# Kernel optimization log

Measured on AMD Instinct MI355X. Metric: run time of the kernel, lower is better.

The kernel has to match this reference:

```python
import jax, jax.numpy as jnp
import numpy as np

N_RUNS, T, N_AGENTS, SENSING = 128, 2048, 16, 7
HIDDEN, OUT = 22, 2


def setup_inputs() -> dict:
    key = jax.random.key(0)
    k_runs, k_comm, k_w1, k_b1, k_w2, k_b2 = jax.random.split(key, 6)
    runs = jax.random.normal(k_runs, (N_RUNS, T, N_AGENTS, SENSING), dtype=jnp.float32)
    # init_comm: zero boundary pads, uniform(0,1) interior, one vector per run
    comm_init = jax.random.uniform(k_comm, (N_RUNS, N_AGENTS + 2), dtype=jnp.float32)
    comm_init = comm_init.at[:, 0].set(0.0).at[:, -1].set(0.0)
    W1 = jax.random.normal(k_w1, (HIDDEN, SENSING + 2), dtype=jnp.float32) * (1.0 / np.sqrt(SENSING + 2))
    b1 = jax.random.normal(k_b1, (HIDDEN,), dtype=jnp.float32) * 0.01
    W2 = jax.random.normal(k_w2, (OUT, HIDDEN), dtype=jnp.float32) * (1.0 / np.sqrt(HIDDEN))
    b2 = jax.random.normal(k_b2, (OUT,), dtype=jnp.float32) * 0.01
    return {"runs": runs, "comm_init": comm_init, "W1": W1, "b1": b1, "W2": W2, "b2": b2}


def reference(runs, comm_init, W1, b1, W2, b2):
    # Sync.sequential: agents processed in index order; agent i reads comm[i]
    # (freshly written by agent i-1) and comm[i+2], then writes comm[i+1].
    n_agents = runs.shape[2]

    def agent_step(carry, i):
        comm, xs_t = carry  # comm: [N+2], xs_t: [N, 7]
        inp = jnp.concatenate([xs_t[i], jnp.stack([comm[i], comm[i + 2]])])  # [9]
        h = jax.nn.relu(W1 @ inp + b1)
        out = W2 @ h + b2  # [2]: (control, new_comm)
        comm = comm.at[i + 1].set(out[1])
        return (comm, xs_t), out[0]

    def time_step(comm, xs_t):
        (comm, _), controls = jax.lax.scan(agent_step, (comm, xs_t), jnp.arange(n_agents))
        return comm, controls  # controls: [N]

    def run_fn(run, comm0):
        # comm persists across timesteps within a run
        _, controls = jax.lax.scan(time_step, comm0, run)
        return controls  # [T, N]

    return jax.vmap(run_fn)(runs, comm_init)  # [n_runs, T, N]
```

## Files before the change

### kernel.cpp

```cpp
#include <hip/hip_runtime.h>

#define NRUNS  128
#define TSTEPS 2048
#define NAG    16
#define SENS   7
#define HID    22

typedef float float2v __attribute__((ext_vector_type(2)));

template<int CTRL>
__device__ __forceinline__ float dpp_mov(float v) {
    return __int_as_float(__builtin_amdgcn_update_dpp(
        0, __float_as_int(v), CTRL, 0xf, 0xf, true));
}

__device__ __forceinline__ float grp_reduce(float v) {
    v += dpp_mov<0xB1>(v);
    v += dpp_mov<0x4E>(v);
    v += dpp_mov<0x141>(v);
    return v;
}

__device__ __forceinline__ float bperm(int byteaddr, float v) {
    return __int_as_float(__builtin_amdgcn_ds_bpermute(byteaddr, __float_as_int(v)));
}

struct RawBlk { float2v v[4][7]; };
struct XpBlk  { float e[4][3]; float o[4][3]; };

__global__ void __launch_bounds__(64, 1) comm_net_kernel(
    const float* __restrict__ runs,
    const float* __restrict__ comm_init,
    const float* __restrict__ W1,
    const float* __restrict__ b1,
    const float* __restrict__ W2,
    const float* __restrict__ b2,
    float* __restrict__ out)
{
    const int run  = blockIdx.x;
    const int lane = threadIdx.x & 63;
    const int g    = lane >> 3;
    const int sub  = lane & 7;
    const bool g0  = (g == 0);
    const bool g7  = (g == 7);

    float w1x[3][SENS], wA[3], wB[3], b1v[3], w20[3], w21[3];
#pragma unroll
    for (int u = 0; u < 3; ++u) {
        int j = sub * 3 + u;
        bool valid = (j < HID);
        int jj = valid ? j : 0;
        float m = valid ? 1.0f : 0.0f;
#pragma unroll
        for (int k = 0; k < SENS; ++k) w1x[u][k] = m * W1[jj * 9 + k];
        wA[u]  = m * W1[jj * 9 + 7];
        wB[u]  = m * W1[jj * 9 + 8];
        b1v[u] = m * b1[jj];
        w20[u] = m * W2[jj];
        w21[u] = m * W2[HID + jj];
    }
    const float b20 = b2[0], b21 = b2[1];

    const int addr_even = ((lane - 8) & 63) * 4;
    const int addr_odd  = ((lane + 8) & 63) * 4;

    const float* ci = comm_init + run * (NAG + 2);
    float prevV = ci[2 * g + 2];
    const float initV_e = ci[2 * g + 1];
    const float initV_o = ci[2 * g + 2];

    const float* pr = runs + (size_t)run * TSTEPS * NAG * SENS;
    float*       po = out  + (size_t)run * TSTEPS * NAG;

    auto xpart_pair = [&](const float2v (&r)[7], float (&ae)[3], float (&ao)[3]) {
#pragma unroll
        for (int u = 0; u < 3; ++u) {
            float e = b1v[u];
            e = fmaf(w1x[u][0], r[0].x, e);
            e = fmaf(w1x[u][1], r[0].y, e);
            e = fmaf(w1x[u][2], r[1].x, e);
            e = fmaf(w1x[u][3], r[1].y, e);
            e = fmaf(w1x[u][4], r[2].x, e);
            e = fmaf(w1x[u][5], r[2].y, e);
            e = fmaf(w1x[u][6], r[3].x, e);
            ae[u] = e;
            float o = b1v[u];
            o = fmaf(w1x[u][0], r[3].y, o);
            o = fmaf(w1x[u][1], r[4].x, o);
            o = fmaf(w1x[u][2], r[4].y, o);
            o = fmaf(w1x[u][3], r[5].x, o);
            o = fmaf(w1x[u][4], r[5].y, o);
            o = fmaf(w1x[u][5], r[6].x, o);
            o = fmaf(w1x[u][6], r[6].y, o);
            ao[u] = o;
        }
    };

    auto substep_even = [&](float xe0, float xe1, float xe2, float& o0out) {
        float cross = bperm(addr_even, prevV);
        float cL = g0 ? 0.f : cross;
        float a0 = fmaxf(fmaf(wA[0], cL, fmaf(wB[0], prevV, xe0)), 0.f);
        float a1 = fmaxf(fmaf(wA[1], cL, fmaf(wB[1], prevV, xe1)), 0.f);
        float a2 = fmaxf(fmaf(wA[2], cL, fmaf(wB[2], prevV, xe2)), 0.f);
        float p0 = w20[0] * a0; p0 = fmaf(w20[1], a1, p0); p0 = fmaf(w20[2], a2, p0);
        float p1 = w21[0] * a0; p1 = fmaf(w21[1], a1, p1); p1 = fmaf(w21[2], a2, p1);
        o0out = grp_reduce(p0) + b20;
        prevV = grp_reduce(p1) + b21;
    };
    auto substep_odd = [&](float xo0, float xo1, float xo2, float& o0out) {
        float cross = bperm(addr_odd, prevV);
        float cR = g7 ? 0.f : cross;
        float a0 = fmaxf(fmaf(wB[0], cR, fmaf(wA[0], prevV, xo0)), 0.f);
        float a1 = fmaxf(fmaf(wB[1], cR, fmaf(wA[1], prevV, xo1)), 0.f);
        float a2 = fmaxf(fmaf(wB[2], cR, fmaf(wA[2], prevV, xo2)), 0.f);
        float p0 = w20[0] * a0; p0 = fmaf(w20[1], a1, p0); p0 = fmaf(w20[2], a2, p0);
        float p1 = w21[0] * a0; p1 = fmaf(w21[1], a1, p1); p1 = fmaf(w21[2], a2, p1);
        o0out = grp_reduce(p0) + b20;
        prevV = grp_reduce(p1) + b21;
    };

    auto ramp_pair = [&](int s) {
        int t  = (s >> 1) - g;
        int tc = t < 0 ? 0 : (t > TSTEPS - 1 ? TSTEPS - 1 : t);
        const float2v* xp = (const float2v*)(pr + ((size_t)tc * NAG + 2 * g) * SENS);
        float2v r[7];
#pragma unroll
        for (int k = 0; k < 7; ++k) r[k] = xp[k];
        float ae[3], ao[3];
        xpart_pair(r, ae, ao);
        bool inr = (t >= 0) && (t < TSTEPS);
        float o0;
        substep_even(ae[0], ae[1], ae[2], o0);
        if (inr) po[(size_t)t * NAG + 2 * g] = o0;
        prevV = (t < 0) ? initV_e : prevV;
        substep_odd(ao[0], ao[1], ao[2], o0);
        if (inr) po[(size_t)t * NAG + 2 * g + 1] = o0;
        prevV = (t < 0) ? initV_o : prevV;
    };

#pragma unroll 1
    for (int s = 0; s <= 14; s += 2) ramp_pair(s);

    const float2v* xv = (const float2v*)(pr + ((size_t)(8 - g) * NAG + 2 * g) * SENS);
    float* oe = po + (size_t)(8 - g) * NAG + 2 * g;

    RawBlk RA, RB;
    XpBlk  P0, P1;

    auto load_blk = [&](RawBlk& R, const float2v* p) {
#pragma unroll
        for (int j = 0; j < 4; ++j)
#pragma unroll
            for (int k = 0; k < 7; ++k)
                R.v[j][k] = p[j * 56 + k];
    };
    auto xpart_blk = [&](XpBlk& P, const RawBlk& R) {
#pragma unroll
        for (int j = 0; j < 4; ++j) xpart_pair(R.v[j], P.e[j], P.o[j]);
    };
    auto process_blk = [&](const XpBlk& P) {
#pragma unroll
        for (int j = 0; j < 4; ++j) {
            float o0;
            substep_even(P.e[j][0], P.e[j][1], P.e[j][2], o0);
            oe[0] = o0;
            substep_odd(P.o[j][0], P.o[j][1], P.o[j][2], o0);
            oe[1] = o0;
            oe += NAG;
        }
    };

    load_blk(RA, xv);
    load_blk(RB, xv + 224);
    xpart_blk(P0, RA);
    load_blk(RA, xv + 2 * 224);

#pragma unroll 1
    for (int bm = 0; bm < 506; bm += 2) {
        xpart_blk(P1, RB);
        load_blk(RB, xv + (size_t)(bm + 3) * 224);
        process_blk(P0);
        xpart_blk(P0, RA);
        load_blk(RA, xv + (size_t)(bm + 4) * 224);
        process_blk(P1);
    }
    xpart_blk(P1, RB);
    load_blk(RB, xv + (size_t)509 * 224);
    process_blk(P0);
    xpart_blk(P0, RA);
    process_blk(P1);
    xpart_blk(P1, RB);
    process_blk(P0);
    process_blk(P1);

#pragma unroll 1
    for (int s = 2 * TSTEPS; s <= 2 * TSTEPS + 12; s += 2) ramp_pair(s);
}

extern "C" void kernel_launch(void* const* d_in, const int* in_sizes, int n_in,
                              void* d_out, int out_size, void* d_ws, size_t ws_size,
                              hipStream_t stream) {
    const float* runs      = (const float*)d_in[0];
    const float* comm_init = (const float*)d_in[1];
    const float* W1        = (const float*)d_in[2];
    const float* b1        = (const float*)d_in[3];
    const float* W2        = (const float*)d_in[4];
    const float* b2        = (const float*)d_in[5];
    float* out = (float*)d_out;

    dim3 grid(NRUNS), block(64);
    hipLaunchKernelGGL(comm_net_kernel, grid, block, 0, stream,
                       runs, comm_init, W1, b1, W2, b2, out);
}
```

Measured before the change: 456.4 us.

## Remap lanes to agent-major layout with packed float2 math and permlane reductions

```diff
diff --git a/kernel.cpp b/kernel.cpp
--- a/kernel.cpp
+++ b/kernel.cpp
@@ -14,19 +14,15 @@
         0, __float_as_int(v), CTRL, 0xf, 0xf, true));
 }
 
-__device__ __forceinline__ float grp_reduce(float v) {
-    v += dpp_mov<0xB1>(v);
-    v += dpp_mov<0x4E>(v);
-    v += dpp_mov<0x141>(v);
-    return v;
-}
-
-__device__ __forceinline__ float bperm(int byteaddr, float v) {
-    return __int_as_float(__builtin_amdgcn_ds_bpermute(byteaddr, __float_as_int(v)));
-}
-
-struct RawBlk { float2v v[4][7]; };
-struct XpBlk  { float e[4][3]; float o[4][3]; };
+__device__ __forceinline__ float grp_sum(float v) {
+    v += dpp_mov<0x128>(v);
+    unsigned u = __float_as_uint(v);
+    auto r = __builtin_amdgcn_permlane32_swap(u, u, false, false);
+    return __uint_as_float(r[0]) + __uint_as_float(r[1]);
+}
+
+struct RawBlk { float2v v[2][7]; };
+struct XpBlk  { float2v e[2][3]; float2v o[2][3]; };
 
 __global__ void __launch_bounds__(64, 1) comm_net_kernel(
     const float* __restrict__ runs,
@@ -39,30 +35,34 @@
 {
     const int run  = blockIdx.x;
     const int lane = threadIdx.x & 63;
-    const int g    = lane >> 3;
-    const int sub  = lane & 7;
-    const bool g0  = (g == 0);
-    const bool g7  = (g == 7);
-
-    float w1x[3][SENS], wA[3], wB[3], b1v[3], w20[3], w21[3];
-#pragma unroll
-    for (int u = 0; u < 3; ++u) {
-        int j = sub * 3 + u;
-        bool valid = (j < HID);
-        int jj = valid ? j : 0;
-        float m = valid ? 1.0f : 0.0f;
-#pragma unroll
-        for (int k = 0; k < SENS; ++k) w1x[u][k] = m * W1[jj * 9 + k];
-        wA[u]  = m * W1[jj * 9 + 7];
-        wB[u]  = m * W1[jj * 9 + 8];
-        b1v[u] = m * b1[jj];
-        w20[u] = m * W2[jj];
-        w21[u] = m * W2[HID + jj];
+    const int g    = lane & 7;
+    const int sub2 = ((lane >> 3) & 1) | ((lane >> 4) & 2);
+    const bool g0 = (g == 0);
+    const bool g7 = (g == 7);
+
+    float2v w1p[3][SENS], b1p[3], wAp[3], wAmp[3], wBp[3], wBmp[3], w20p[3], w21p[3];
+#pragma unroll
+    for (int u2 = 0; u2 < 3; ++u2) {
+#pragma unroll
+        for (int h = 0; h < 2; ++h) {
+            int j = sub2 * 6 + u2 * 2 + h;
+            bool valid = (j < HID);
+            int jj = valid ? j : 0;
+            float m = valid ? 1.0f : 0.0f;
+#pragma unroll
+            for (int k = 0; k < SENS; ++k) w1p[u2][k][h] = m * W1[jj * 9 + k];
+            float wa = m * W1[jj * 9 + 7];
+            float wb = m * W1[jj * 9 + 8];
+            wAp[u2][h]  = wa;
+            wAmp[u2][h] = g0 ? 0.f : wa;
+            wBp[u2][h]  = wb;
+            wBmp[u2][h] = g7 ? 0.f : wb;
+            b1p[u2][h]  = m * b1[jj];
+            w20p[u2][h] = m * W2[jj];
+            w21p[u2][h] = m * W2[HID + jj];
+        }
     }
     const float b20 = b2[0], b21 = b2[1];
-
-    const int addr_even = ((lane - 8) & 63) * 4;
-    const int addr_odd  = ((lane + 8) & 63) * 4;
 
     const float* ci = comm_init + run * (NAG + 2);
     float prevV = ci[2 * g + 2];
@@ -72,51 +72,57 @@
     const float* pr = runs + (size_t)run * TSTEPS * NAG * SENS;
     float*       po = out  + (size_t)run * TSTEPS * NAG;
 
-    auto xpart_pair = [&](const float2v (&r)[7], float (&ae)[3], float (&ao)[3]) {
-#pragma unroll
-        for (int u = 0; u < 3; ++u) {
-            float e = b1v[u];
-            e = fmaf(w1x[u][0], r[0].x, e);
-            e = fmaf(w1x[u][1], r[0].y, e);
-            e = fmaf(w1x[u][2], r[1].x, e);
-            e = fmaf(w1x[u][3], r[1].y, e);
-            e = fmaf(w1x[u][4], r[2].x, e);
-            e = fmaf(w1x[u][5], r[2].y, e);
-            e = fmaf(w1x[u][6], r[3].x, e);
-            ae[u] = e;
-            float o = b1v[u];
-            o = fmaf(w1x[u][0], r[3].y, o);
-            o = fmaf(w1x[u][1], r[4].x, o);
-            o = fmaf(w1x[u][2], r[4].y, o);
-            o = fmaf(w1x[u][3], r[5].x, o);
-            o = fmaf(w1x[u][4], r[5].y, o);
-            o = fmaf(w1x[u][5], r[6].x, o);
-            o = fmaf(w1x[u][6], r[6].y, o);
-            ao[u] = o;
+    auto xpart_pair = [&](const float2v (&r)[7], float2v (&ae)[3], float2v (&ao)[3]) {
+#pragma unroll
+        for (int u2 = 0; u2 < 3; ++u2) {
+            float2v e = b1p[u2];
+            e = w1p[u2][0] * (float2v){r[0].x, r[0].x} + e;
+            e = w1p[u2][1] * (float2v){r[0].y, r[0].y} + e;
+            e = w1p[u2][2] * (float2v){r[1].x, r[1].x} + e;
+            e = w1p[u2][3] * (float2v){r[1].y, r[1].y} + e;
+            e = w1p[u2][4] * (float2v){r[2].x, r[2].x} + e;
+            e = w1p[u2][5] * (float2v){r[2].y, r[2].y} + e;
+            e = w1p[u2][6] * (float2v){r[3].x, r[3].x} + e;
+            ae[u2] = e;
+            float2v o = b1p[u2];
+            o = w1p[u2][0] * (float2v){r[3].y, r[3].y} + o;
+            o = w1p[u2][1] * (float2v){r[4].x, r[4].x} + o;
+            o = w1p[u2][2] * (float2v){r[4].y, r[4].y} + o;
+            o = w1p[u2][3] * (float2v){r[5].x, r[5].x} + o;
+            o = w1p[u2][4] * (float2v){r[5].y, r[5].y} + o;
+            o = w1p[u2][5] * (float2v){r[6].x, r[6].x} + o;
+            o = w1p[u2][6] * (float2v){r[6].y, r[6].y} + o;
+            ao[u2] = o;
         }
     };
 
-    auto substep_even = [&](float xe0, float xe1, float xe2, float& o0out) {
-        float cross = bperm(addr_even, prevV);
-        float cL = g0 ? 0.f : cross;
-        float a0 = fmaxf(fmaf(wA[0], cL, fmaf(wB[0], prevV, xe0)), 0.f);
-        float a1 = fmaxf(fmaf(wA[1], cL, fmaf(wB[1], prevV, xe1)), 0.f);
-        float a2 = fmaxf(fmaf(wA[2], cL, fmaf(wB[2], prevV, xe2)), 0.f);
-        float p0 = w20[0] * a0; p0 = fmaf(w20[1], a1, p0); p0 = fmaf(w20[2], a2, p0);
-        float p1 = w21[0] * a0; p1 = fmaf(w21[1], a1, p1); p1 = fmaf(w21[2], a2, p1);
-        o0out = grp_reduce(p0) + b20;
-        prevV = grp_reduce(p1) + b21;
-    };
-    auto substep_odd = [&](float xo0, float xo1, float xo2, float& o0out) {
-        float cross = bperm(addr_odd, prevV);
-        float cR = g7 ? 0.f : cross;
-        float a0 = fmaxf(fmaf(wB[0], cR, fmaf(wA[0], prevV, xo0)), 0.f);
-        float a1 = fmaxf(fmaf(wB[1], cR, fmaf(wA[1], prevV, xo1)), 0.f);
-        float a2 = fmaxf(fmaf(wB[2], cR, fmaf(wA[2], prevV, xo2)), 0.f);
-        float p0 = w20[0] * a0; p0 = fmaf(w20[1], a1, p0); p0 = fmaf(w20[2], a2, p0);
-        float p1 = w21[0] * a0; p1 = fmaf(w21[1], a1, p1); p1 = fmaf(w21[2], a2, p1);
-        o0out = grp_reduce(p0) + b20;
-        prevV = grp_reduce(p1) + b21;
+    auto substep_even = [&](const float2v (&xe)[3], float& o0out) {
+        float cL = dpp_mov<0x111>(prevV);
+        float2v cL2 = {cL, cL}, pV2 = {prevV, prevV};
+        float2v a0 = wAmp[0] * cL2 + (wBp[0] * pV2 + xe[0]);
+        float2v a1 = wAmp[1] * cL2 + (wBp[1] * pV2 + xe[1]);
+        float2v a2 = wAmp[2] * cL2 + (wBp[2] * pV2 + xe[2]);
+        a0.x = fmaxf(a0.x, 0.f); a0.y = fmaxf(a0.y, 0.f);
+        a1.x = fmaxf(a1.x, 0.f); a1.y = fmaxf(a1.y, 0.f);
+        a2.x = fmaxf(a2.x, 0.f); a2.y = fmaxf(a2.y, 0.f);
+        float2v q0 = w20p[0] * a0; q0 = w20p[1] * a1 + q0; q0 = w20p[2] * a2 + q0;
+        float2v q1 = w21p[0] * a0; q1 = w21p[1] * a1 + q1; q1 = w21p[2] * a2 + q1;
+        o0out = grp_sum(q0.x + q0.y) + b20;
+        prevV = grp_sum(q1.x + q1.y) + b21;
+    };
+    auto substep_odd = [&](const float2v (&xo)[3], float& o0out) {
+        float cR = dpp_mov<0x101>(prevV);
+        float2v cR2 = {cR, cR}, pV2 = {prevV, prevV};
+        float2v a0 = wBmp[0] * cR2 + (wAp[0] * pV2 + xo[0]);
+        float2v a1 = wBmp[1] * cR2 + (wAp[1] * pV2 + xo[1]);
+        float2v a2 = wBmp[2] * cR2 + (wAp[2] * pV2 + xo[2]);
+        a0.x = fmaxf(a0.x, 0.f); a0.y = fmaxf(a0.y, 0.f);
+        a1.x = fmaxf(a1.x, 0.f); a1.y = fmaxf(a1.y, 0.f);
+        a2.x = fmaxf(a2.x, 0.f); a2.y = fmaxf(a2.y, 0.f);
+        float2v q0 = w20p[0] * a0; q0 = w20p[1] * a1 + q0; q0 = w20p[2] * a2 + q0;
+        float2v q1 = w21p[0] * a0; q1 = w21p[1] * a1 + q1; q1 = w21p[2] * a2 + q1;
+        o0out = grp_sum(q0.x + q0.y) + b20;
+        prevV = grp_sum(q1.x + q1.y) + b21;
     };
 
     auto ramp_pair = [&](int s) {
@@ -126,14 +132,14 @@
         float2v r[7];
 #pragma unroll
         for (int k = 0; k < 7; ++k) r[k] = xp[k];
-        float ae[3], ao[3];
+        float2v ae[3], ao[3];
         xpart_pair(r, ae, ao);
         bool inr = (t >= 0) && (t < TSTEPS);
         float o0;
-        substep_even(ae[0], ae[1], ae[2], o0);
+        substep_even(ae, o0);
         if (inr) po[(size_t)t * NAG + 2 * g] = o0;
         prevV = (t < 0) ? initV_e : prevV;
-        substep_odd(ao[0], ao[1], ao[2], o0);
+        substep_odd(ao, o0);
         if (inr) po[(size_t)t * NAG + 2 * g + 1] = o0;
         prevV = (t < 0) ? initV_o : prevV;
     };
@@ -149,43 +155,43 @@
 
     auto load_blk = [&](RawBlk& R, const float2v* p) {
 #pragma unroll
-        for (int j = 0; j < 4; ++j)
+        for (int j = 0; j < 2; ++j)
 #pragma unroll
             for (int k = 0; k < 7; ++k)
                 R.v[j][k] = p[j * 56 + k];
     };
     auto xpart_blk = [&](XpBlk& P, const RawBlk& R) {
 #pragma unroll
-        for (int j = 0; j < 4; ++j) xpart_pair(R.v[j], P.e[j], P.o[j]);
+        for (int j = 0; j < 2; ++j) xpart_pair(R.v[j], P.e[j], P.o[j]);
     };
     auto process_blk = [&](const XpBlk& P) {
 #pragma unroll
-        for (int j = 0; j < 4; ++j) {
+        for (int j = 0; j < 2; ++j) {
             float o0;
-            substep_even(P.e[j][0], P.e[j][1], P.e[j][2], o0);
+            substep_even(P.e[j], o0);
             oe[0] = o0;
-            substep_odd(P.o[j][0], P.o[j][1], P.o[j][2], o0);
+            substep_odd(P.o[j], o0);
             oe[1] = o0;
             oe += NAG;
         }
     };
 
     load_blk(RA, xv);
-    load_blk(RB, xv + 224);
+    load_blk(RB, xv + 112);
     xpart_blk(P0, RA);
-    load_blk(RA, xv + 2 * 224);
+    load_blk(RA, xv + 2 * 112);
 
 #pragma unroll 1
-    for (int bm = 0; bm < 506; bm += 2) {
+    for (int bm = 0; bm < 1016; bm += 2) {
         xpart_blk(P1, RB);
-        load_blk(RB, xv + (size_t)(bm + 3) * 224);
+        load_blk(RB, xv + (size_t)(bm + 3) * 112);
         process_blk(P0);
         xpart_blk(P0, RA);
-        load_blk(RA, xv + (size_t)(bm + 4) * 224);
+        load_blk(RA, xv + (size_t)(bm + 4) * 112);
         process_blk(P1);
     }
     xpart_blk(P1, RB);
-    load_blk(RB, xv + (size_t)509 * 224);
+    load_blk(RB, xv + (size_t)1019 * 112);
     process_blk(P0);
     xpart_blk(P0, RA);
     process_blk(P1);
```

Measured after the change: 496.6 us. +8.8%, slower.

## Precompute input projection in a parallel fp16 pre-pass, redistribute hidden units across lanes

Applied to the files above, without the earlier changes.

```diff
diff --git a/kernel.cpp b/kernel.cpp
--- a/kernel.cpp
+++ b/kernel.cpp
@@ -5,8 +5,11 @@
 #define NAG    16
 #define SENS   7
 #define HID    22
+#define HP     24
+#define HPRE_BYTES ((size_t)NRUNS * TSTEPS * NAG * HP * 2)
 
 typedef float float2v __attribute__((ext_vector_type(2)));
+typedef _Float16 half2v __attribute__((ext_vector_type(2)));
 
 template<int CTRL>
 __device__ __forceinline__ float dpp_mov(float v) {
@@ -14,27 +17,204 @@
         0, __float_as_int(v), CTRL, 0xf, 0xf, true));
 }
 
-__device__ __forceinline__ float grp_reduce(float v) {
+__device__ __forceinline__ float grp_sum_r(float v) {
+    v += dpp_mov<0x128>(v);
+    unsigned u = __float_as_uint(v);
+    auto r = __builtin_amdgcn_permlane32_swap(u, u, false, false);
+    return __uint_as_float(r[0]) + __uint_as_float(r[1]);
+}
+
+__global__ void __launch_bounds__(256) hpre_kernel(
+    const float* __restrict__ runs, const float* __restrict__ W1,
+    const float* __restrict__ b1, _Float16* __restrict__ hpre)
+{
+    const int tid = blockIdx.x * 256 + threadIdx.x;
+    const int s8  = tid & 7;
+    const int rb  = tid >> 3;
+    float w[3][SENS], bb[3];
+#pragma unroll
+    for (int u = 0; u < 3; ++u) {
+        int j = s8 * 3 + u; bool valid = j < HID; int jj = valid ? j : 0;
+        float m = valid ? 1.f : 0.f;
+#pragma unroll
+        for (int k = 0; k < SENS; ++k) w[u][k] = m * W1[jj * 9 + k];
+        bb[u] = m * b1[jj];
+    }
+#pragma unroll 1
+    for (int q = 0; q < 64; ++q) {
+        long r = (long)rb + (long)q * 65536;
+        const float* x = runs + r * SENS;
+        float x0=x[0],x1=x[1],x2=x[2],x3=x[3],x4=x[4],x5=x[5],x6=x[6];
+        _Float16* hw = hpre + r * HP + s8 * 3;
+#pragma unroll
+        for (int u = 0; u < 3; ++u) {
+            float a = bb[u];
+            a = fmaf(w[u][0], x0, a); a = fmaf(w[u][1], x1, a);
+            a = fmaf(w[u][2], x2, a); a = fmaf(w[u][3], x3, a);
+            a = fmaf(w[u][4], x4, a); a = fmaf(w[u][5], x5, a);
+            a = fmaf(w[u][6], x6, a);
+            hw[u] = (_Float16)a;
+        }
+    }
+}
+
+struct HBlk { half2v h[2][6]; };
+
+__global__ void __launch_bounds__(64, 1) comm_net_kernel(
+    const half2v* __restrict__ hpre2,
+    const float* __restrict__ W1,
+    const float* __restrict__ W2,
+    const float* __restrict__ b2,
+    const float* __restrict__ comm_init,
+    float* __restrict__ out)
+{
+    const int run  = blockIdx.x;
+    const int lane = threadIdx.x & 63;
+    const int g    = lane & 7;
+    const int sub2 = ((lane >> 3) & 1) | ((lane >> 4) & 2);
+    const bool g0  = (g == 0);
+    const bool g7  = (g == 7);
+
+    float wA[6], wAm[6], wB[6], wBm[6], w20[6], w21[6];
+#pragma unroll
+    for (int v = 0; v < 6; ++v) {
+        int j = sub2 * 6 + v; bool valid = j < HID; int jj = valid ? j : 0;
+        float m = valid ? 1.f : 0.f;
+        float wa = m * W1[jj * 9 + 7];
+        float wb = m * W1[jj * 9 + 8];
+        wA[v] = wa; wAm[v] = g0 ? 0.f : wa;
+        wB[v] = wb; wBm[v] = g7 ? 0.f : wb;
+        w20[v] = m * W2[jj];
+        w21[v] = m * W2[HID + jj];
+    }
+    const float b20s = (sub2 == 0) ? b2[0] : 0.f;
+    const float b21s = (sub2 == 0) ? b2[1] : 0.f;
+
+    const float* ci = comm_init + run * (NAG + 2);
+    float prevV = ci[2 * g + 2];
+    const float initV_e = ci[2 * g + 1];
+    const float initV_o = ci[2 * g + 2];
+
+    const half2v* hp2 = hpre2 + (long)run * (TSTEPS * NAG * HP / 2);
+    float*        po  = out   + (size_t)run * TSTEPS * NAG;
+
+    auto substep_even = [&](const float (&h)[6], float& o0out) {
+        float cL = dpp_mov<0x111>(prevV);
+        float a[6];
+#pragma unroll
+        for (int v = 0; v < 6; ++v)
+            a[v] = fmaxf(fmaf(wAm[v], cL, fmaf(wB[v], prevV, h[v])), 0.f);
+        float q0a = fmaf(w20[1], a[1], fmaf(w20[0], a[0], b20s));
+        float q0b = fmaf(w20[3], a[3], w20[2] * a[2]);
+        float q0c = fmaf(w20[5], a[5], w20[4] * a[4]);
+        float q1a = fmaf(w21[1], a[1], fmaf(w21[0], a[0], b21s));
+        float q1b = fmaf(w21[3], a[3], w21[2] * a[2]);
+        float q1c = fmaf(w21[5], a[5], w21[4] * a[4]);
+        prevV = grp_sum_r((q1a + q1b) + q1c);
+        o0out = grp_sum_r((q0a + q0b) + q0c);
+    };
+    auto substep_odd = [&](const float (&h)[6], float& o0out) {
+        float cR = dpp_mov<0x101>(prevV);
+        float a[6];
+#pragma unroll
+        for (int v = 0; v < 6; ++v)
+            a[v] = fmaxf(fmaf(wBm[v], cR, fmaf(wA[v], prevV, h[v])), 0.f);
+        float q0a = fmaf(w20[1], a[1], fmaf(w20[0], a[0], b20s));
+        float q0b = fmaf(w20[3], a[3], w20[2] * a[2]);
+        float q0c = fmaf(w20[5], a[5], w20[4] * a[4]);
+        float q1a = fmaf(w21[1], a[1], fmaf(w21[0], a[0], b21s));
+        float q1b = fmaf(w21[3], a[3], w21[2] * a[2]);
+        float q1c = fmaf(w21[5], a[5], w21[4] * a[4]);
+        prevV = grp_sum_r((q1a + q1b) + q1c);
+        o0out = grp_sum_r((q0a + q0b) + q0c);
+    };
+
+    auto ramp_pair = [&](int s) {
+        int t  = (s >> 1) - g;
+        int tc = t < 0 ? 0 : (t > TSTEPS - 1 ? TSTEPS - 1 : t);
+        long db = (long)tc * 192 + (2 * g) * 12 + sub2 * 3;
+        float he[6], ho[6];
+#pragma unroll
+        for (int k = 0; k < 3; ++k) {
+            half2v e = hp2[db + k], o = hp2[db + 12 + k];
+            he[2*k] = (float)e.x; he[2*k+1] = (float)e.y;
+            ho[2*k] = (float)o.x; ho[2*k+1] = (float)o.y;
+        }
+        bool inr = (t >= 0) && (t < TSTEPS);
+        float o0;
+        substep_even(he, o0);
+        if (inr) po[(size_t)t * NAG + 2 * g] = o0;
+        prevV = (t < 0) ? initV_e : prevV;
+        substep_odd(ho, o0);
+        if (inr) po[(size_t)t * NAG + 2 * g + 1] = o0;
+        prevV = (t < 0) ? initV_o : prevV;
+    };
+
+#pragma unroll 1
+    for (int s = 0; s <= 14; s += 2) ramp_pair(s);
+
+    const long db0 = ((long)(8 - g) * NAG + 2 * g) * 12 + sub2 * 3;
+    float* oe = po + (size_t)(8 - g) * NAG + 2 * g;
+
+    auto load_blk = [&](HBlk& H, long db) {
+#pragma unroll
+        for (int j = 0; j < 2; ++j)
+#pragma unroll
+            for (int k = 0; k < 3; ++k) {
+                H.h[j][k]     = hp2[db + j * 192 + k];
+                H.h[j][3 + k] = hp2[db + j * 192 + 12 + k];
+            }
+    };
+    auto process_blk = [&](const HBlk& H) {
+#pragma unroll
+        for (int j = 0; j < 2; ++j) {
+            float he[6], ho[6];
+#pragma unroll
+            for (int k = 0; k < 3; ++k) {
+                he[2*k] = (float)H.h[j][k].x;     he[2*k+1] = (float)H.h[j][k].y;
+                ho[2*k] = (float)H.h[j][3+k].x;   ho[2*k+1] = (float)H.h[j][3+k].y;
+            }
+            float o0;
+            substep_even(he, o0); oe[0] = o0;
+            substep_odd (ho, o0); oe[1] = o0;
+            oe += NAG;
+        }
+    };
+
+    HBlk HA, HB, HC, HD;
+    load_blk(HA, db0);
+    load_blk(HB, db0 + 384);
+    load_blk(HC, db0 + 768);
+    load_blk(HD, db0 + 1152);
+#pragma unroll 1
+    for (int bm = 0; bm < 1016; bm += 4) {
+        process_blk(HA); load_blk(HA, db0 + (long)(bm + 4) * 384);
+        process_blk(HB); load_blk(HB, db0 + (long)(bm + 5) * 384);
+        process_blk(HC); load_blk(HC, db0 + (long)(bm + 6) * 384);
+        process_blk(HD); load_blk(HD, db0 + (long)(bm + 7) * 384);
+    }
+    process_blk(HA); process_blk(HB); process_blk(HC); process_blk(HD);
+
+#pragma unroll 1
+    for (int s = 2 * TSTEPS; s <= 2 * TSTEPS + 12; s += 2) ramp_pair(s);
+}
+
+__device__ __forceinline__ float grp_reduce_fb(float v) {
     v += dpp_mov<0xB1>(v);
     v += dpp_mov<0x4E>(v);
     v += dpp_mov<0x141>(v);
     return v;
 }
-
-__device__ __forceinline__ float bperm(int byteaddr, float v) {
+__device__ __forceinline__ float bperm_fb(int byteaddr, float v) {
     return __int_as_float(__builtin_amdgcn_ds_bpermute(byteaddr, __float_as_int(v)));
 }
-
 struct RawBlk { float2v v[4][7]; };
 struct XpBlk  { float e[4][3]; float o[4][3]; };
 
-__global__ void __launch_bounds__(64, 1) comm_net_kernel(
-    const float* __restrict__ runs,
-    const float* __restrict__ comm_init,
-    const float* __restrict__ W1,
-    const float* __restrict__ b1,
-    const float* __restrict__ W2,
-    const float* __restrict__ b2,
+__global__ void __launch_bounds__(64, 1) comm_net_fb(
+    const float* __restrict__ runs, const float* __restrict__ comm_init,
+    const float* __restrict__ W1, const float* __restrict__ b1,
+    const float* __restrict__ W2, const float* __restrict__ b2,
     float* __restrict__ out)
 {
     const int run  = blockIdx.x;
@@ -43,82 +223,64 @@
     const int sub  = lane & 7;
     const bool g0  = (g == 0);
     const bool g7  = (g == 7);
-
     float w1x[3][SENS], wA[3], wB[3], b1v[3], w20[3], w21[3];
 #pragma unroll
     for (int u = 0; u < 3; ++u) {
-        int j = sub * 3 + u;
-        bool valid = (j < HID);
-        int jj = valid ? j : 0;
+        int j = sub * 3 + u; bool valid = (j < HID); int jj = valid ? j : 0;
         float m = valid ? 1.0f : 0.0f;
 #pragma unroll
         for (int k = 0; k < SENS; ++k) w1x[u][k] = m * W1[jj * 9 + k];
-        wA[u]  = m * W1[jj * 9 + 7];
-        wB[u]  = m * W1[jj * 9 + 8];
-        b1v[u] = m * b1[jj];
-        w20[u] = m * W2[jj];
-        w21[u] = m * W2[HID + jj];
+        wA[u] = m * W1[jj * 9 + 7]; wB[u] = m * W1[jj * 9 + 8];
+        b1v[u] = m * b1[jj]; w20[u] = m * W2[jj]; w21[u] = m * W2[HID + jj];
     }
     const float b20 = b2[0], b21 = b2[1];
-
     const int addr_even = ((lane - 8) & 63) * 4;
     const int addr_odd  = ((lane + 8) & 63) * 4;
-
     const float* ci = comm_init + run * (NAG + 2);
     float prevV = ci[2 * g + 2];
     const float initV_e = ci[2 * g + 1];
     const float initV_o = ci[2 * g + 2];
-
     const float* pr = runs + (size_t)run * TSTEPS * NAG * SENS;
     float*       po = out  + (size_t)run * TSTEPS * NAG;
-
     auto xpart_pair = [&](const float2v (&r)[7], float (&ae)[3], float (&ao)[3]) {
 #pragma unroll
         for (int u = 0; u < 3; ++u) {
             float e = b1v[u];
-            e = fmaf(w1x[u][0], r[0].x, e);
-            e = fmaf(w1x[u][1], r[0].y, e);
-            e = fmaf(w1x[u][2], r[1].x, e);
-            e = fmaf(w1x[u][3], r[1].y, e);
-            e = fmaf(w1x[u][4], r[2].x, e);
-            e = fmaf(w1x[u][5], r[2].y, e);
+            e = fmaf(w1x[u][0], r[0].x, e); e = fmaf(w1x[u][1], r[0].y, e);
+            e = fmaf(w1x[u][2], r[1].x, e); e = fmaf(w1x[u][3], r[1].y, e);
+            e = fmaf(w1x[u][4], r[2].x, e); e = fmaf(w1x[u][5], r[2].y, e);
             e = fmaf(w1x[u][6], r[3].x, e);
             ae[u] = e;
             float o = b1v[u];
-            o = fmaf(w1x[u][0], r[3].y, o);
-            o = fmaf(w1x[u][1], r[4].x, o);
-            o = fmaf(w1x[u][2], r[4].y, o);
-            o = fmaf(w1x[u][3], r[5].x, o);
-            o = fmaf(w1x[u][4], r[5].y, o);
-            o = fmaf(w1x[u][5], r[6].x, o);
+            o = fmaf(w1x[u][0], r[3].y, o); o = fmaf(w1x[u][1], r[4].x, o);
+            o = fmaf(w1x[u][2], r[4].y, o); o = fmaf(w1x[u][3], r[5].x, o);
+            o = fmaf(w1x[u][4], r[5].y, o); o = fmaf(w1x[u][5], r[6].x, o);
             o = fmaf(w1x[u][6], r[6].y, o);
             ao[u] = o;
         }
     };
-
-    auto substep_even = [&](float xe0, float xe1, float xe2, float& o0out) {
-        float cross = bperm(addr_even, prevV);
+    auto substep_even = [&](float x0, float x1, float x2, float& o0out) {
+        float cross = bperm_fb(addr_even, prevV);
         float cL = g0 ? 0.f : cross;
-        float a0 = fmaxf(fmaf(wA[0], cL, fmaf(wB[0], prevV, xe0)), 0.f);
-        float a1 = fmaxf(fmaf(wA[1], cL, fmaf(wB[1], prevV, xe1)), 0.f);
-        float a2 = fmaxf(fmaf(wA[2], cL, fmaf(wB[2], prevV, xe2)), 0.f);
-        float p0 = w20[0] * a0; p0 = fmaf(w20[1], a1, p0); p0 = fmaf(w20[2], a2, p0);
-        float p1 = w21[0] * a0; p1 = fmaf(w21[1], a1, p1); p1 = fmaf(w21[2], a2, p1);
-        o0out = grp_reduce(p0) + b20;
-        prevV = grp_reduce(p1) + b21;
-    };
-    auto substep_odd = [&](float xo0, float xo1, float xo2, float& o0out) {
-        float cross = bperm(addr_odd, prevV);
+        float a0 = fmaxf(fmaf(wA[0], cL, fmaf(wB[0], prevV, x0)), 0.f);
+        float a1 = fmaxf(fmaf(wA[1], cL, fmaf(wB[1], prevV, x1)), 0.f);
+        float a2 = fmaxf(fmaf(wA[2], cL, fmaf(wB[2], prevV, x2)), 0.f);
+        float p0 = w20[0]*a0; p0 = fmaf(w20[1],a1,p0); p0 = fmaf(w20[2],a2,p0);
+        float p1 = w21[0]*a0; p1 = fmaf(w21[1],a1,p1); p1 = fmaf(w21[2],a2,p1);
+        o0out = grp_reduce_fb(p0) + b20;
+        prevV = grp_reduce_fb(p1) + b21;
+    };
+    auto substep_odd = [&](float x0, float x1, float x2, float& o0out) {
+        float cross = bperm_fb(addr_odd, prevV);
         float cR = g7 ? 0.f : cross;
-        float a0 = fmaxf(fmaf(wB[0], cR, fmaf(wA[0], prevV, xo0)), 0.f);
-        float a1 = fmaxf(fmaf(wB[1], cR, fmaf(wA[1], prevV, xo1)), 0.f);
-        float a2 = fmaxf(fmaf(wB[2], cR, fmaf(wA[2], prevV, xo2)), 0.f);
-        float p0 = w20[0] * a0; p0 = fmaf(w20[1], a1, p0); p0 = fmaf(w20[2], a2, p0);
-        float p1 = w21[0] * a0; p1 = fmaf(w21[1], a1, p1); p1 = fmaf(w21[2], a2, p1);
-        o0out = grp_reduce(p0) + b20;
-        prevV = grp_reduce(p1) + b21;
-    };
-
+        float a0 = fmaxf(fmaf(wB[0], cR, fmaf(wA[0], prevV, x0)), 0.f);
+        float a1 = fmaxf(fmaf(wB[1], cR, fmaf(wA[1], prevV, x1)), 0.f);
+        float a2 = fmaxf(fmaf(wB[2], cR, fmaf(wA[2], prevV, x2)), 0.f);
+        float p0 = w20[0]*a0; p0 = fmaf(w20[1],a1,p0); p0 = fmaf(w20[2],a2,p0);
+        float p1 = w21[0]*a0; p1 = fmaf(w21[1],a1,p1); p1 = fmaf(w21[2],a2,p1);
+        o0out = grp_reduce_fb(p0) + b20;
+        prevV = grp_reduce_fb(p1) + b21;
+    };
     auto ramp_pair = [&](int s) {
         int t  = (s >> 1) - g;
         int tc = t < 0 ? 0 : (t > TSTEPS - 1 ? TSTEPS - 1 : t);
@@ -137,22 +299,16 @@
         if (inr) po[(size_t)t * NAG + 2 * g + 1] = o0;
         prevV = (t < 0) ? initV_o : prevV;
     };
-
 #pragma unroll 1
     for (int s = 0; s <= 14; s += 2) ramp_pair(s);
-
     const float2v* xv = (const float2v*)(pr + ((size_t)(8 - g) * NAG + 2 * g) * SENS);
     float* oe = po + (size_t)(8 - g) * NAG + 2 * g;
-
-    RawBlk RA, RB;
-    XpBlk  P0, P1;
-
+    RawBlk RA, RB; XpBlk P0, P1;
     auto load_blk = [&](RawBlk& R, const float2v* p) {
 #pragma unroll
         for (int j = 0; j < 4; ++j)
 #pragma unroll
-            for (int k = 0; k < 7; ++k)
-                R.v[j][k] = p[j * 56 + k];
+            for (int k = 0; k < 7; ++k) R.v[j][k] = p[j * 56 + k];
     };
     auto xpart_blk = [&](XpBlk& P, const RawBlk& R) {
 #pragma unroll
@@ -162,37 +318,24 @@
 #pragma unroll
         for (int j = 0; j < 4; ++j) {
             float o0;
-            substep_even(P.e[j][0], P.e[j][1], P.e[j][2], o0);
-            oe[0] = o0;
-            substep_odd(P.o[j][0], P.o[j][1], P.o[j][2], o0);
-            oe[1] = o0;
+            substep_even(P.e[j][0], P.e[j][1], P.e[j][2], o0); oe[0] = o0;
+            substep_odd (P.o[j][0], P.o[j][1], P.o[j][2], o0); oe[1] = o0;
             oe += NAG;
         }
     };
-
-    load_blk(RA, xv);
-    load_blk(RB, xv + 224);
-    xpart_blk(P0, RA);
-    load_blk(RA, xv + 2 * 224);
-
+    load_blk(RA, xv); load_blk(RB, xv + 224);
+    xpart_blk(P0, RA); load_blk(RA, xv + 2 * 224);
 #pragma unroll 1
     for (int bm = 0; bm < 506; bm += 2) {
-        xpart_blk(P1, RB);
-        load_blk(RB, xv + (size_t)(bm + 3) * 224);
+        xpart_blk(P1, RB); load_blk(RB, xv + (size_t)(bm + 3) * 224);
         process_blk(P0);
-        xpart_blk(P0, RA);
-        load_blk(RA, xv + (size_t)(bm + 4) * 224);
+        xpart_blk(P0, RA); load_blk(RA, xv + (size_t)(bm + 4) * 224);
         process_blk(P1);
     }
-    xpart_blk(P1, RB);
-    load_blk(RB, xv + (size_t)509 * 224);
+    xpart_blk(P1, RB); load_blk(RB, xv + (size_t)509 * 224);
     process_blk(P0);
-    xpart_blk(P0, RA);
-    process_blk(P1);
-    xpart_blk(P1, RB);
-    process_blk(P0);
-    process_blk(P1);
-
+    xpart_blk(P0, RA); process_blk(P1);
+    xpart_blk(P1, RB); process_blk(P0); process_blk(P1);
 #pragma unroll 1
     for (int s = 2 * TSTEPS; s <= 2 * TSTEPS + 12; s += 2) ramp_pair(s);
 }
@@ -208,7 +351,14 @@
     const float* b2        = (const float*)d_in[5];
     float* out = (float*)d_out;
 
-    dim3 grid(NRUNS), block(64);
-    hipLaunchKernelGGL(comm_net_kernel, grid, block, 0, stream,
-                       runs, comm_init, W1, b1, W2, b2, out);
-}
+    if (ws_size >= HPRE_BYTES) {
+        _Float16* hpre = (_Float16*)d_ws;
+        hipLaunchKernelGGL(hpre_kernel, dim3(2048), dim3(256), 0, stream,
+                           runs, W1, b1, hpre);
+        hipLaunchKernelGGL(comm_net_kernel, dim3(NRUNS), dim3(64), 0, stream,
+                           (const half2v*)hpre, W1, W2, b2, comm_init, out);
+    } else {
+        hipLaunchKernelGGL(comm_net_fb, dim3(NRUNS), dim3(64), 0, stream,
+                           runs, comm_init, W1, b1, W2, b2, out);
+    }
+}
```

New measurement: 514.0 us. 1.13x slower.
